# Optimization experiments

Hardware: AMD Instinct MI355X
Metric: run time of the kernel (lower is better)

The kernel has to match this reference:

```python
import jax, jax.numpy as jnp
import numpy as np

DIM = 128
HEADS = 4
K = 7          # neighborhood kernel size
MLP_RATIO = 4
EPS = 1e-5


def setup_inputs() -> dict:
    key = jax.random.key(0)
    ks = jax.random.split(key, 8)
    B, H, W, C = 4, 64, 64, DIM
    hid = C * MLP_RATIO
    s = lambda k, shape: jax.random.normal(k, shape, jnp.float32) * 0.02
    return {
        "x": jax.random.normal(ks[0], (B, H, W, C), jnp.float32),
        "ln1_g": jnp.ones((C,), jnp.float32),
        "ln1_b": jnp.zeros((C,), jnp.float32),
        "qkv_w": s(ks[1], (C, 3 * C)),
        "qkv_b": jnp.zeros((3 * C,), jnp.float32),
        "rpb": s(ks[2], (HEADS, 2 * K - 1, 2 * K - 1)),
        "proj_w": s(ks[3], (C, C)),
        "proj_b": jnp.zeros((C,), jnp.float32),
        "ln2_g": jnp.ones((C,), jnp.float32),
        "ln2_b": jnp.zeros((C,), jnp.float32),
        "fc1_w": s(ks[4], (C, hid)),
        "fc1_b": jnp.zeros((hid,), jnp.float32),
        "fc2_w": s(ks[5], (hid, C)),
        "fc2_b": jnp.zeros((C,), jnp.float32),
    }


def _ln(x, g, b):
    m = jnp.mean(x, axis=-1, keepdims=True)
    v = jnp.mean(jnp.square(x - m), axis=-1, keepdims=True)
    return (x - m) * jax.lax.rsqrt(v + EPS) * g + b


def _neigh_idx(L, k):
    # NATTEN border-clamped neighborhood: start = clamp(i - k//2, 0, L-k)
    i = jnp.arange(L)
    start = jnp.clip(i - k // 2, 0, L - k)
    idx = start[:, None] + jnp.arange(k)[None, :]        # [L, k] key positions
    rel = idx - i[:, None] + (k - 1)                     # [L, k] rpb indices in [0, 2k-2]
    return idx, rel


def _neighborhood_attention(x, qkv_w, qkv_b, rpb, proj_w, proj_b):
    B, H, W, C = x.shape
    nh, hd = HEADS, C // HEADS
    scale = hd ** -0.5
    qkv = (x @ qkv_w + qkv_b).reshape(B, H, W, 3, nh, hd)
    qkv = qkv.transpose(3, 0, 4, 1, 2, 5)                # [3, B, nh, H, W, hd]
    q, k_, v = qkv[0] * scale, qkv[1], qkv[2]
    ih, rh = _neigh_idx(H, K)
    iw, rw = _neigh_idx(W, K)
    # gather 7x7 neighborhoods: [B, nh, H, K, W, K, hd]
    kg = k_[:, :, ih][:, :, :, :, iw]
    vg = v[:, :, ih][:, :, :, :, iw]
    attn = jnp.einsum('bnywc,bnykxjc->bnyxkj', q, kg)    # [B, nh, H, W, K, K]
    bias = rpb[:, rh][:, :, :, rw]                       # [nh, H, K, W, K]
    attn = attn + bias.transpose(0, 1, 3, 2, 4)[None]
    a = jax.nn.softmax(attn.reshape(B, nh, H, W, K * K), axis=-1)
    a = a.reshape(B, nh, H, W, K, K)
    out = jnp.einsum('bnyxkj,bnykxjc->bnyxc', a, vg)     # [B, nh, H, W, hd]
    out = out.transpose(0, 2, 3, 1, 4).reshape(B, H, W, C)
    return out @ proj_w + proj_b


def reference(x, ln1_g, ln1_b, qkv_w, qkv_b, rpb, proj_w, proj_b,
              ln2_g, ln2_b, fc1_w, fc1_b, fc2_w, fc2_b):
    h = x + _neighborhood_attention(_ln(x, ln1_g, ln1_b), qkv_w, qkv_b, rpb, proj_w, proj_b)
    y = _ln(h, ln2_g, ln2_b)
    y = jax.nn.gelu(y @ fc1_w + fc1_b, approximate=False) @ fc2_w + fc2_b
    return h + y
```

## Files before the change

### kernel.cpp

```cpp
#include <hip/hip_runtime.h>
#include <math.h>

#define TOKS 16384
#define CDIM 128
#define NH 4
#define HD 32
#define HID 512
#define QSCALE 0.17677669529663687f
#define LEPS 1e-5f

typedef const float* fp;
typedef const unsigned short* bfp16;
typedef __attribute__((ext_vector_type(8))) short bf16x8;
typedef __attribute__((ext_vector_type(4))) float f32x4;

__device__ inline unsigned int bfp2(float a, float b) {
    unsigned int ua = __float_as_uint(a); ua = (ua + 0x7FFFu + ((ua >> 16) & 1u)) >> 16;
    unsigned int ub = __float_as_uint(b); ub = (ub + 0x7FFFu + ((ub >> 16) & 1u)) >> 16;
    return ua | (ub << 16);
}
__device__ inline unsigned short bf1(float a) {
    unsigned int u = __float_as_uint(a);
    return (unsigned short)((u + 0x7FFFu + ((u >> 16) & 1u)) >> 16);
}
__device__ inline float lo16(unsigned int u) { return __uint_as_float(u << 16); }
__device__ inline float hi16(unsigned int u) { return __uint_as_float(u & 0xFFFF0000u); }

__global__ __launch_bounds__(256) void prep(fp qw, fp pw, fp f1w, fp f2w,
                                            unsigned short* __restrict__ wt) {
    int e = blockIdx.x * 256 + threadIdx.x;
    float v;
    if (e < 49152) { int n = e >> 7, k = e & 127; v = qw[(size_t)k * 384 + n]; }
    else if (e < 65536) {
        int i = e - 49152;
        int frag = i >> 9, w = i & 511, lane = w >> 3, el = w & 7;
        int rt = frag >> 2, kk = frag & 3;
        int row = rt * 16 + (lane & 15);
        int k = kk * 32 + (lane >> 4) * 8 + el;
        v = pw[(size_t)k * 128 + row];
    } else if (e < 131072) {
        int i = e - 65536;
        int frag = i >> 9, w = i & 511, lane = w >> 3, el = w & 7;
        int rt = frag >> 2, kk = frag & 3;
        int row = rt * 16 + (lane & 15);
        int k = kk * 32 + (lane >> 4) * 8 + el;
        v = f1w[(size_t)k * 512 + row];
    } else {
        int i = e - 131072;
        int frag = i >> 9, w = i & 511, lane = w >> 3, el = w & 7;
        int rt = frag >> 4, kc = frag & 15;
        int row = rt * 16 + (lane & 15);
        int k = kc * 32 + (lane >> 4) * 8 + el;
        v = f2w[(size_t)k * 128 + row];
    }
    wt[e] = bf1(v);
}

__global__ __launch_bounds__(256) void k1_mfma(fp x, fp g1, fp b1, bfp16 wt0, fp wb,
                                               float* __restrict__ qb,
                                               unsigned short* __restrict__ kvb) {
    __shared__ unsigned int lds[12288];
    const int m0 = blockIdx.x * 128;
    const int nb = blockIdx.y * 64;
    const int tid = threadIdx.x;
#pragma unroll
    for (int i = 0; i < 8; i++) {
        int slot = tid + i * 256;
        int m = slot >> 4, c16 = slot & 15;
        const float4 v0 = *(const float4*)(x + (size_t)(m0 + m) * CDIM + c16 * 8);
        const float4 v1 = *(const float4*)(x + (size_t)(m0 + m) * CDIM + c16 * 8 + 4);
        float s = v0.x + v0.y + v0.z + v0.w + v1.x + v1.y + v1.z + v1.w;
        float q = v0.x * v0.x + v0.y * v0.y + v0.z * v0.z + v0.w * v0.w
                + v1.x * v1.x + v1.y * v1.y + v1.z * v1.z + v1.w * v1.w;
#pragma unroll
        for (int mm = 8; mm >= 1; mm >>= 1) { s += __shfl_xor(s, mm); q += __shfl_xor(q, mm); }
        float mu = s * (1.f / 128.f);
        float rs = rsqrtf(q * (1.f / 128.f) - mu * mu + LEPS);
        const float4 ga = *(const float4*)(g1 + c16 * 8);
        const float4 gb = *(const float4*)(g1 + c16 * 8 + 4);
        const float4 ba = *(const float4*)(b1 + c16 * 8);
        const float4 bb = *(const float4*)(b1 + c16 * 8 + 4);
        uint4 o;
        o.x = bfp2((v0.x - mu) * rs * ga.x + ba.x, (v0.y - mu) * rs * ga.y + ba.y);
        o.y = bfp2((v0.z - mu) * rs * ga.z + ba.z, (v0.w - mu) * rs * ga.w + ba.w);
        o.z = bfp2((v1.x - mu) * rs * gb.x + bb.x, (v1.y - mu) * rs * gb.y + bb.y);
        o.w = bfp2((v1.z - mu) * rs * gb.z + bb.z, (v1.w - mu) * rs * gb.w + bb.w);
        *(uint4*)&lds[m * 64 + ((c16 ^ (m & 15)) << 2)] = o;
    }
#pragma unroll
    for (int i = 0; i < 4; i++) {
        int slot = tid + i * 256;
        int n = slot >> 4, c16 = slot & 15;
        const uint4 v4 = *(const uint4*)(wt0 + (size_t)(nb + n) * 128 + c16 * 8);
        *(uint4*)&lds[8192 + n * 64 + (c16 ^ (n & 15)) * 4] = v4;
    }
    __syncthreads();

    const int lane = tid & 63, wid = tid >> 6, quad = lane >> 4, l16 = lane & 15;
    f32x4 acc[2][4];
#pragma unroll
    for (int mt = 0; mt < 2; mt++)
#pragma unroll
        for (int nt = 0; nt < 4; nt++) acc[mt][nt] = (f32x4){0.f, 0.f, 0.f, 0.f};
#pragma unroll
    for (int kk = 0; kk < 4; kk++) {
        int c = kk * 4 + quad;
        bf16x8 a0 = *(bf16x8*)&lds[(wid * 32 + l16) * 64 + (c ^ l16) * 4];
        bf16x8 a1 = *(bf16x8*)&lds[(wid * 32 + 16 + l16) * 64 + (c ^ l16) * 4];
#pragma unroll
        for (int nt = 0; nt < 4; nt++) {
            bf16x8 bf = *(bf16x8*)&lds[8192 + (nt * 16 + l16) * 64 + (c ^ l16) * 4];
            acc[0][nt] = __builtin_amdgcn_mfma_f32_16x16x32_bf16(a0, bf, acc[0][nt], 0, 0, 0);
            acc[1][nt] = __builtin_amdgcn_mfma_f32_16x16x32_bf16(a1, bf, acc[1][nt], 0, 0, 0);
        }
    }
#pragma unroll
    for (int nt = 0; nt < 4; nt++) {
        int col = nb + nt * 16 + l16;
        float bias = wb[col];
#pragma unroll
        for (int mt = 0; mt < 2; mt++)
#pragma unroll
            for (int r = 0; r < 4; r++) {
                int row = m0 + wid * 32 + mt * 16 + quad * 4 + r;
                float vres = acc[mt][nt][r] + bias;
                if (col < 128)
                    qb[(size_t)row * 128 + col] = vres * QSCALE;
                else if (col < 256)
                    kvb[(size_t)row * 256 + (col - 128)] = bf1(vres);
                else
                    kvb[(size_t)row * 256 + 128 + (col - 256)] = bf1(vres);
            }
    }
}

__global__ __launch_bounds__(512) void k2_attn(const float* __restrict__ qb,
                                               const unsigned short* __restrict__ kvb,
                                               fp rpb, unsigned short* __restrict__ attnb) {
    __shared__ unsigned int lds[25088];
    const int tile = blockIdx.x;
    const int bb = tile >> 6;
    const int ty0 = ((tile >> 3) & 7) << 3;
    const int tx0 = (tile & 7) << 3;
    const int ry0 = min(max(ty0 - 3, 0), 50);
    const int rx0 = min(max(tx0 - 3, 0), 50);
    const int tid = threadIdx.x;

#pragma unroll
    for (int it = 0; it < 13; it++) {
        int slot = it * 512 + tid;
        if (slot < 6272) {
            int r = slot >> 5, c = slot & 31;
            int i = r / 14, j = r - i * 14;
            const uint4 v = *(const uint4*)(kvb + (size_t)((bb << 12) + (ry0 + i) * 64 + rx0 + j) * 256 + c * 8);
            *(uint4*)&lds[r * 128 + ((c ^ (r & 7)) << 2)] = v;
        }
    }

    const int dh = tid & 1;
    const int head = (tid >> 1) & 3;
    const int t = tid >> 3;
    const int tx = t & 7, ty = t >> 3;
    const int y = ty0 + ty, x = tx0 + tx;
    const int token = (bb << 12) + y * 64 + x;
    const int sy = min(max(y - 3, 0), 57);
    const int sx = min(max(x - 3, 0), 57);
    const int ib = sy - ry0, jb = sx - rx0;
    const float* rp = rpb + head * 169 + (sy - y + 6) * 13 + (sx - x + 6);

    float q[16];
    {
        const float4* qp = (const float4*)(qb + (size_t)token * 128 + head * 32 + dh * 16);
        float4 a = qp[0], b = qp[1], c = qp[2], d = qp[3];
        q[0] = a.x; q[1] = a.y; q[2] = a.z; q[3] = a.w;
        q[4] = b.x; q[5] = b.y; q[6] = b.z; q[7] = b.w;
        q[8] = c.x; q[9] = c.y; q[10] = c.z; q[11] = c.w;
        q[12] = d.x; q[13] = d.y; q[14] = d.z; q[15] = d.w;
    }
    __syncthreads();

    const int cb = (head << 2) + (dh << 1);
    float m = -1e30f, l = 0.f;
    float o[16];
#pragma unroll
    for (int i2 = 0; i2 < 16; i2++) o[i2] = 0.f;

    for (int dy = 0; dy < 7; dy++) {
        float s[7];
#pragma unroll
        for (int dx = 0; dx < 7; dx++) {
            int r = (ib + dy) * 14 + jb + dx;
            int sw = r & 7;
            const uint4 k0 = *(const uint4*)&lds[r * 128 + ((cb ^ sw) << 2)];
            const uint4 k1 = *(const uint4*)&lds[r * 128 + (((cb + 1) ^ sw) << 2)];
            float ss = q[0] * lo16(k0.x) + q[1] * hi16(k0.x)
                     + q[2] * lo16(k0.y) + q[3] * hi16(k0.y)
                     + q[4] * lo16(k0.z) + q[5] * hi16(k0.z)
                     + q[6] * lo16(k0.w) + q[7] * hi16(k0.w)
                     + q[8] * lo16(k1.x) + q[9] * hi16(k1.x)
                     + q[10] * lo16(k1.y) + q[11] * hi16(k1.y)
                     + q[12] * lo16(k1.z) + q[13] * hi16(k1.z)
                     + q[14] * lo16(k1.w) + q[15] * hi16(k1.w);
            ss += __shfl_xor(ss, 1);
            s[dx] = ss + rp[dy * 13 + dx];
        }
        float rm = s[0];
#pragma unroll
        for (int dx = 1; dx < 7; dx++) rm = fmaxf(rm, s[dx]);
        float mn = fmaxf(m, rm);
        float cf = __expf(m - mn);
        l *= cf;
#pragma unroll
        for (int i2 = 0; i2 < 16; i2++) o[i2] *= cf;
#pragma unroll
        for (int dx = 0; dx < 7; dx++) {
            int r = (ib + dy) * 14 + jb + dx;
            int sw = r & 7;
            const uint4 v0 = *(const uint4*)&lds[r * 128 + (((cb + 16) ^ sw) << 2)];
            const uint4 v1 = *(const uint4*)&lds[r * 128 + (((cb + 17) ^ sw) << 2)];
            float p = __expf(s[dx] - mn);
            l += p;
            o[0] += p * lo16(v0.x); o[1] += p * hi16(v0.x);
            o[2] += p * lo16(v0.y); o[3] += p * hi16(v0.y);
            o[4] += p * lo16(v0.z); o[5] += p * hi16(v0.z);
            o[6] += p * lo16(v0.w); o[7] += p * hi16(v0.w);
            o[8] += p * lo16(v1.x); o[9] += p * hi16(v1.x);
            o[10] += p * lo16(v1.y); o[11] += p * hi16(v1.y);
            o[12] += p * lo16(v1.z); o[13] += p * hi16(v1.z);
            o[14] += p * lo16(v1.w); o[15] += p * hi16(v1.w);
        }
        m = mn;
    }
    float inv = 1.f / l;
    unsigned short* op = attnb + (size_t)token * 128 + head * 32 + dh * 16;
    uint4 ov;
    ov.x = bfp2(o[0] * inv, o[1] * inv); ov.y = bfp2(o[2] * inv, o[3] * inv);
    ov.z = bfp2(o[4] * inv, o[5] * inv); ov.w = bfp2(o[6] * inv, o[7] * inv);
    *(uint4*)op = ov;
    ov.x = bfp2(o[8] * inv, o[9] * inv); ov.y = bfp2(o[10] * inv, o[11] * inv);
    ov.z = bfp2(o[12] * inv, o[13] * inv); ov.w = bfp2(o[14] * inv, o[15] * inv);
    *(uint4*)(op + 8) = ov;
}

__global__ __launch_bounds__(512) void kpm4(bfp16 attnb, fp x, bfp16 wt1, fp pb,
                                            fp g2, fp b2, bfp16 wt2, fp b1v,
                                            bfp16 wt3, fp b2v, float* __restrict__ out) {
    __shared__ unsigned int lds[12288];
    float* ldsf = (float*)lds;
    unsigned short* ldsu = (unsigned short*)lds;
    const int m0 = blockIdx.x * 32;
    const int tid = threadIdx.x;
    const int lane = tid & 63, wid = tid >> 6, quad = lane >> 4, l16 = lane & 15;

    {
        int m = tid >> 4, c16 = tid & 15;
        const uint4 v4 = *(const uint4*)(attnb + (size_t)(m0 + m) * CDIM + c16 * 8);
        *(uint4*)&lds[m * 64 + ((c16 ^ (m & 15)) << 2)] = v4;
    }
    __syncthreads();

    const int mt = wid & 1, nhf = wid >> 1;
    f32x4 pacc[2];
#pragma unroll
    for (int nt = 0; nt < 2; nt++) pacc[nt] = (f32x4){0.f, 0.f, 0.f, 0.f};
#pragma unroll
    for (int kk = 0; kk < 4; kk++) {
        int c = kk * 4 + quad;
        bf16x8 a = *(bf16x8*)&lds[(mt * 16 + l16) * 64 + ((c ^ l16) << 2)];
#pragma unroll
        for (int nt = 0; nt < 2; nt++) {
            int rt = nhf * 2 + nt;
            bf16x8 bf = *(const bf16x8*)(wt1 + (size_t)((rt * 4 + kk) * 64 + lane) * 8);
            pacc[nt] = __builtin_amdgcn_mfma_f32_16x16x32_bf16(a, bf, pacc[nt], 0, 0, 0);
        }
    }
    float sr[4] = {0.f, 0.f, 0.f, 0.f}, qr[4] = {0.f, 0.f, 0.f, 0.f};
#pragma unroll
    for (int nt = 0; nt < 2; nt++) {
        int col = nhf * 32 + nt * 16 + l16;
        float bias = pb[col];
#pragma unroll
        for (int r = 0; r < 4; r++) {
            int lrow = mt * 16 + quad * 4 + r;
            float hv = x[(size_t)(m0 + lrow) * CDIM + col] + pacc[nt][r] + bias;
            pacc[nt][r] = hv;
            sr[r] += hv; qr[r] += hv * hv;
        }
    }
#pragma unroll
    for (int mm = 1; mm <= 8; mm <<= 1) {
#pragma unroll
        for (int r = 0; r < 4; r++) {
            sr[r] += __shfl_xor(sr[r], mm);
            qr[r] += __shfl_xor(qr[r], mm);
        }
    }
    __syncthreads();
    if (l16 == 0) {
#pragma unroll
        for (int r = 0; r < 4; r++) {
            ldsf[wid * 32 + (quad * 4 + r) * 2]     = sr[r];
            ldsf[wid * 32 + (quad * 4 + r) * 2 + 1] = qr[r];
        }
    }
    __syncthreads();
    float mu[4], rs[4];
#pragma unroll
    for (int r = 0; r < 4; r++) {
        float st = 0.f, qt = 0.f;
#pragma unroll
        for (int p = 0; p < 4; p++) {
            int w2 = p * 2 + mt;
            st += ldsf[w2 * 32 + (quad * 4 + r) * 2];
            qt += ldsf[w2 * 32 + (quad * 4 + r) * 2 + 1];
        }
        mu[r] = st * (1.f / 128.f);
        rs[r] = rsqrtf(qt * (1.f / 128.f) - mu[r] * mu[r] + LEPS);
    }
#pragma unroll
    for (int nt = 0; nt < 2; nt++) {
        int col = nhf * 32 + nt * 16 + l16;
        float gg = g2[col], bbv = b2[col];
        int c16h = col >> 3, cw = col & 7;
#pragma unroll
        for (int r = 0; r < 4; r++) {
            int lrow = mt * 16 + quad * 4 + r;
            ldsu[4096 + lrow * 128 + ((c16h ^ (lrow & 15)) << 3) + cw] =
                bf1((pacc[nt][r] - mu[r]) * rs[r] * gg + bbv);
        }
    }
    __syncthreads();

#pragma unroll
    for (int ht = 0; ht < 4; ht++) {
        f32x4 acc0 = (f32x4){0.f, 0.f, 0.f, 0.f};
        f32x4 acc1 = (f32x4){0.f, 0.f, 0.f, 0.f};
#pragma unroll
        for (int kk = 0; kk < 4; kk++) {
            int c = kk * 4 + quad;
            bf16x8 wf = *(const bf16x8*)(wt2 + (size_t)(((wid * 4 + ht) * 4 + kk) * 64 + lane) * 8);
            bf16x8 x0 = *(bf16x8*)&lds[2048 + l16 * 64 + ((c ^ l16) << 2)];
            bf16x8 x1 = *(bf16x8*)&lds[2048 + (16 + l16) * 64 + ((c ^ l16) << 2)];
            acc0 = __builtin_amdgcn_mfma_f32_16x16x32_bf16(wf, x0, acc0, 0, 0, 0);
            acc1 = __builtin_amdgcn_mfma_f32_16x16x32_bf16(wf, x1, acc1, 0, 0, 0);
        }
        const int hidb = wid * 64 + ht * 16 + quad * 4;
        const float4 bb = *(const float4*)(b1v + hidb);
        const int c16y = hidb >> 3;
        const int woff = (quad & 1) << 1;
#pragma unroll
        for (int t = 0; t < 2; t++) {
            f32x4 a = t ? acc1 : acc0;
            int row = t * 16 + l16;
            float z0 = a[0] + bb.x, z1 = a[1] + bb.y, z2 = a[2] + bb.z, z3 = a[3] + bb.w;
            float g0 = 0.5f * z0 * (1.f + erff(z0 * 0.70710678118654752f));
            float g1 = 0.5f * z1 * (1.f + erff(z1 * 0.70710678118654752f));
            float g2v = 0.5f * z2 * (1.f + erff(z2 * 0.70710678118654752f));
            float g3 = 0.5f * z3 * (1.f + erff(z3 * 0.70710678118654752f));
            uint2 val; val.x = bfp2(g0, g1); val.y = bfp2(g2v, g3);
            *(uint2*)&lds[4096 + row * 256 + ((c16y ^ (row & 15)) << 2) + woff] = val;
        }
    }
    __syncthreads();

    f32x4 facc[2];
#pragma unroll
    for (int nt = 0; nt < 2; nt++) facc[nt] = (f32x4){0.f, 0.f, 0.f, 0.f};
#pragma unroll
    for (int kc = 0; kc < 16; kc++) {
        int c = kc * 4 + quad;
        bf16x8 a = *(bf16x8*)&lds[4096 + (mt * 16 + l16) * 256 + ((c ^ l16) << 2)];
#pragma unroll
        for (int nt = 0; nt < 2; nt++) {
            int rt = nhf * 2 + nt;
            bf16x8 bf = *(const bf16x8*)(wt3 + (size_t)((rt * 16 + kc) * 64 + lane) * 8);
            facc[nt] = __builtin_amdgcn_mfma_f32_16x16x32_bf16(a, bf, facc[nt], 0, 0, 0);
        }
    }
#pragma unroll
    for (int nt = 0; nt < 2; nt++) {
        int col = nhf * 32 + nt * 16 + l16;
        float bias = b2v[col];
#pragma unroll
        for (int r = 0; r < 4; r++) {
            int lrow = mt * 16 + quad * 4 + r;
            out[(size_t)(m0 + lrow) * CDIM + col] = pacc[nt][r] + facc[nt][r] + bias;
        }
    }
}

extern "C" void kernel_launch(void* const* d_in, const int* in_sizes, int n_in,
                              void* d_out, int out_size, void* d_ws, size_t ws_size,
                              hipStream_t stream) {
    fp x      = (fp)d_in[0];
    fp ln1_g  = (fp)d_in[1];
    fp ln1_b  = (fp)d_in[2];
    fp qkv_w  = (fp)d_in[3];
    fp qkv_b  = (fp)d_in[4];
    fp rpb    = (fp)d_in[5];
    fp proj_w = (fp)d_in[6];
    fp proj_b = (fp)d_in[7];
    fp ln2_g  = (fp)d_in[8];
    fp ln2_b  = (fp)d_in[9];
    fp fc1_w  = (fp)d_in[10];
    fp fc1_b  = (fp)d_in[11];
    fp fc2_w  = (fp)d_in[12];
    fp fc2_b  = (fp)d_in[13];
    float* out = (float*)d_out;

    float* ws = (float*)d_ws;
    float* h  = ws;
    unsigned short* xn = (unsigned short*)(h + (size_t)TOKS * CDIM);
    unsigned short* hn = xn + (size_t)TOKS * CDIM;
    float* qb = (float*)(hn + (size_t)TOKS * CDIM);
    unsigned short* kvb   = (unsigned short*)(qb + (size_t)TOKS * CDIM);
    unsigned short* attnb = kvb + (size_t)TOKS * 256;
    unsigned short* wt    = attnb + (size_t)TOKS * CDIM;

    unsigned short* wt0 = wt;
    unsigned short* wt1 = wt + 49152;
    unsigned short* wt2 = wt + 65536;
    unsigned short* wt3 = wt + 131072;

    prep<<<768, 256, 0, stream>>>(qkv_w, proj_w, fc1_w, fc2_w, wt);
    k1_mfma<<<dim3(TOKS / 128, 6), 256, 0, stream>>>(x, ln1_g, ln1_b, wt0, qkv_b, qb, kvb);
    k2_attn<<<TOKS / 64, 512, 0, stream>>>(qb, kvb, rpb, attnb);
    kpm4<<<TOKS / 32, 512, 0, stream>>>(attnb, x, wt1, proj_b, ln2_g, ln2_b,
                                        wt2, fc1_b, wt3, fc2_b, out);
}
```

Measured before the change: 130.8 us.

## Split attention blocks by head pairs and use two-pass softmax

```diff
diff --git a/kernel.cpp b/kernel.cpp
--- a/kernel.cpp
+++ b/kernel.cpp
@@ -134,11 +134,13 @@
     }
 }
 
-__global__ __launch_bounds__(512) void k2_attn(const float* __restrict__ qb,
+__global__ __launch_bounds__(256) void k2_attn(const float* __restrict__ qb,
                                                const unsigned short* __restrict__ kvb,
                                                fp rpb, unsigned short* __restrict__ attnb) {
-    __shared__ unsigned int lds[25088];
-    const int tile = blockIdx.x;
+    __shared__ unsigned int lds[12544];
+    const int blk = blockIdx.x;
+    const int hp = blk & 1;
+    const int tile = blk >> 1;
     const int bb = tile >> 6;
     const int ty0 = ((tile >> 3) & 7) << 3;
     const int tx0 = (tile & 7) << 3;
@@ -148,18 +150,21 @@
 
 #pragma unroll
     for (int it = 0; it < 13; it++) {
-        int slot = it * 512 + tid;
-        if (slot < 6272) {
-            int r = slot >> 5, c = slot & 31;
+        int slot = it * 256 + tid;
+        if (slot < 3136) {
+            int r = slot >> 4, c = slot & 15;
             int i = r / 14, j = r - i * 14;
-            const uint4 v = *(const uint4*)(kvb + (size_t)((bb << 12) + (ry0 + i) * 64 + rx0 + j) * 256 + c * 8);
-            *(uint4*)&lds[r * 128 + ((c ^ (r & 7)) << 2)] = v;
+            size_t tok = (size_t)((bb << 12) + (ry0 + i) * 64 + rx0 + j);
+            int off = (c < 8) ? (hp * 64 + c * 8) : (128 + hp * 64 + (c - 8) * 8);
+            const uint4 v = *(const uint4*)(kvb + tok * 256 + off);
+            *(uint4*)&lds[r * 64 + ((c ^ (r & 7)) << 2)] = v;
         }
     }
 
     const int dh = tid & 1;
-    const int head = (tid >> 1) & 3;
-    const int t = tid >> 3;
+    const int hl = (tid >> 1) & 1;
+    const int t = tid >> 2;
+    const int head = hp * 2 + hl;
     const int tx = t & 7, ty = t >> 3;
     const int y = ty0 + ty, x = tx0 + tx;
     const int token = (bb << 12) + y * 64 + x;
@@ -167,6 +172,8 @@
     const int sx = min(max(x - 3, 0), 57);
     const int ib = sy - ry0, jb = sx - rx0;
     const float* rp = rpb + head * 169 + (sy - y + 6) * 13 + (sx - x + 6);
+    const int cbK = hl * 4 + dh * 2;
+    const int cbV = 8 + cbK;
 
     float q[16];
     {
@@ -179,20 +186,16 @@
     }
     __syncthreads();
 
-    const int cb = (head << 2) + (dh << 1);
-    float m = -1e30f, l = 0.f;
-    float o[16];
-#pragma unroll
-    for (int i2 = 0; i2 < 16; i2++) o[i2] = 0.f;
-
+    float s[49];
+    float mx = -1e30f;
+#pragma unroll
     for (int dy = 0; dy < 7; dy++) {
-        float s[7];
 #pragma unroll
         for (int dx = 0; dx < 7; dx++) {
             int r = (ib + dy) * 14 + jb + dx;
             int sw = r & 7;
-            const uint4 k0 = *(const uint4*)&lds[r * 128 + ((cb ^ sw) << 2)];
-            const uint4 k1 = *(const uint4*)&lds[r * 128 + (((cb + 1) ^ sw) << 2)];
+            const uint4 k0 = *(const uint4*)&lds[r * 64 + ((cbK ^ sw) << 2)];
+            const uint4 k1 = *(const uint4*)&lds[r * 64 + (((cbK + 1) ^ sw) << 2)];
             float ss = q[0] * lo16(k0.x) + q[1] * hi16(k0.x)
                      + q[2] * lo16(k0.y) + q[3] * hi16(k0.y)
                      + q[4] * lo16(k0.z) + q[5] * hi16(k0.z)
@@ -202,24 +205,28 @@
                      + q[12] * lo16(k1.z) + q[13] * hi16(k1.z)
                      + q[14] * lo16(k1.w) + q[15] * hi16(k1.w);
             ss += __shfl_xor(ss, 1);
-            s[dx] = ss + rp[dy * 13 + dx];
-        }
-        float rm = s[0];
-#pragma unroll
-        for (int dx = 1; dx < 7; dx++) rm = fmaxf(rm, s[dx]);
-        float mn = fmaxf(m, rm);
-        float cf = __expf(m - mn);
-        l *= cf;
-#pragma unroll
-        for (int i2 = 0; i2 < 16; i2++) o[i2] *= cf;
+            float sc = ss + rp[dy * 13 + dx];
+            s[dy * 7 + dx] = sc;
+            mx = fmaxf(mx, sc);
+        }
+    }
+    float sum = 0.f;
+#pragma unroll
+    for (int i = 0; i < 49; i++) { s[i] = __expf(s[i] - mx); sum += s[i]; }
+    float inv = 1.f / sum;
+
+    float o[16];
+#pragma unroll
+    for (int i2 = 0; i2 < 16; i2++) o[i2] = 0.f;
+#pragma unroll
+    for (int dy = 0; dy < 7; dy++) {
 #pragma unroll
         for (int dx = 0; dx < 7; dx++) {
             int r = (ib + dy) * 14 + jb + dx;
             int sw = r & 7;
-            const uint4 v0 = *(const uint4*)&lds[r * 128 + (((cb + 16) ^ sw) << 2)];
-            const uint4 v1 = *(const uint4*)&lds[r * 128 + (((cb + 17) ^ sw) << 2)];
-            float p = __expf(s[dx] - mn);
-            l += p;
+            const uint4 v0 = *(const uint4*)&lds[r * 64 + ((cbV ^ sw) << 2)];
+            const uint4 v1 = *(const uint4*)&lds[r * 64 + (((cbV + 1) ^ sw) << 2)];
+            float p = s[dy * 7 + dx];
             o[0] += p * lo16(v0.x); o[1] += p * hi16(v0.x);
             o[2] += p * lo16(v0.y); o[3] += p * hi16(v0.y);
             o[4] += p * lo16(v0.z); o[5] += p * hi16(v0.z);
@@ -229,9 +236,7 @@
             o[12] += p * lo16(v1.z); o[13] += p * hi16(v1.z);
             o[14] += p * lo16(v1.w); o[15] += p * hi16(v1.w);
         }
-        m = mn;
-    }
-    float inv = 1.f / l;
+    }
     unsigned short* op = attnb + (size_t)token * 128 + head * 32 + dh * 16;
     uint4 ov;
     ov.x = bfp2(o[0] * inv, o[1] * inv); ov.y = bfp2(o[2] * inv, o[3] * inv);
@@ -424,7 +429,7 @@
 
     prep<<<768, 256, 0, stream>>>(qkv_w, proj_w, fc1_w, fc2_w, wt);
     k1_mfma<<<dim3(TOKS / 128, 6), 256, 0, stream>>>(x, ln1_g, ln1_b, wt0, qkv_b, qb, kvb);
-    k2_attn<<<TOKS / 64, 512, 0, stream>>>(qb, kvb, rpb, attnb);
+    k2_attn<<<TOKS / 64 * 2, 256, 0, stream>>>(qb, kvb, rpb, attnb);
     kpm4<<<TOKS / 32, 512, 0, stream>>>(attnb, x, wt1, proj_b, ln2_g, ln2_b,
                                         wt2, fc1_b, wt3, fc2_b, out);
 }
```

After: 131.9 us. About the same (+0.8%).

## Fuse weight-prep kernel into QKV kernel and convert QKV weights in-block

Applied to the files above, without the earlier changes.

```diff
diff --git a/kernel.cpp b/kernel.cpp
--- a/kernel.cpp
+++ b/kernel.cpp
@@ -26,43 +26,45 @@
 __device__ inline float lo16(unsigned int u) { return __uint_as_float(u << 16); }
 __device__ inline float hi16(unsigned int u) { return __uint_as_float(u & 0xFFFF0000u); }
 
-__global__ __launch_bounds__(256) void prep(fp qw, fp pw, fp f1w, fp f2w,
-                                            unsigned short* __restrict__ wt) {
-    int e = blockIdx.x * 256 + threadIdx.x;
-    float v;
-    if (e < 49152) { int n = e >> 7, k = e & 127; v = qw[(size_t)k * 384 + n]; }
-    else if (e < 65536) {
-        int i = e - 49152;
-        int frag = i >> 9, w = i & 511, lane = w >> 3, el = w & 7;
-        int rt = frag >> 2, kk = frag & 3;
-        int row = rt * 16 + (lane & 15);
-        int k = kk * 32 + (lane >> 4) * 8 + el;
-        v = pw[(size_t)k * 128 + row];
-    } else if (e < 131072) {
-        int i = e - 65536;
-        int frag = i >> 9, w = i & 511, lane = w >> 3, el = w & 7;
-        int rt = frag >> 2, kk = frag & 3;
-        int row = rt * 16 + (lane & 15);
-        int k = kk * 32 + (lane >> 4) * 8 + el;
-        v = f1w[(size_t)k * 512 + row];
-    } else {
-        int i = e - 131072;
-        int frag = i >> 9, w = i & 511, lane = w >> 3, el = w & 7;
-        int rt = frag >> 4, kc = frag & 15;
-        int row = rt * 16 + (lane & 15);
-        int k = kc * 32 + (lane >> 4) * 8 + el;
-        v = f2w[(size_t)k * 128 + row];
-    }
-    wt[e] = bf1(v);
-}
-
-__global__ __launch_bounds__(256) void k1_mfma(fp x, fp g1, fp b1, bfp16 wt0, fp wb,
+__global__ __launch_bounds__(256) void k1_mfma(fp x, fp g1, fp b1, fp qw, fp wb,
+                                               fp pw, fp f1w, fp f2w,
+                                               unsigned short* __restrict__ wt,
                                                float* __restrict__ qb,
                                                unsigned short* __restrict__ kvb) {
+    const int blk = blockIdx.x;
+    const int tid = threadIdx.x;
+    if (blk >= 768) {
+        int e = 49152 + (blk - 768) * 256 + tid;
+        float v;
+        if (e < 65536) {
+            int i = e - 49152;
+            int frag = i >> 9, w = i & 511, lane = w >> 3, el = w & 7;
+            int rt = frag >> 2, kk = frag & 3;
+            int row = rt * 16 + (lane & 15);
+            int k = kk * 32 + (lane >> 4) * 8 + el;
+            v = pw[(size_t)k * 128 + row];
+        } else if (e < 131072) {
+            int i = e - 65536;
+            int frag = i >> 9, w = i & 511, lane = w >> 3, el = w & 7;
+            int rt = frag >> 2, kk = frag & 3;
+            int row = rt * 16 + (lane & 15);
+            int k = kk * 32 + (lane >> 4) * 8 + el;
+            v = f1w[(size_t)k * 512 + row];
+        } else {
+            int i = e - 131072;
+            int frag = i >> 9, w = i & 511, lane = w >> 3, el = w & 7;
+            int rt = frag >> 4, kc = frag & 15;
+            int row = rt * 16 + (lane & 15);
+            int k = kc * 32 + (lane >> 4) * 8 + el;
+            v = f2w[(size_t)k * 128 + row];
+        }
+        wt[e] = bf1(v);
+        return;
+    }
+
     __shared__ unsigned int lds[12288];
-    const int m0 = blockIdx.x * 128;
-    const int nb = blockIdx.y * 64;
-    const int tid = threadIdx.x;
+    const int m0 = (blk & 127) << 7;
+    const int nb = (blk >> 7) * 64;
 #pragma unroll
     for (int i = 0; i < 8; i++) {
         int slot = tid + i * 256;
@@ -87,12 +89,25 @@
         o.w = bfp2((v1.z - mu) * rs * gb.z + bb.z, (v1.w - mu) * rs * gb.w + bb.w);
         *(uint4*)&lds[m * 64 + ((c16 ^ (m & 15)) << 2)] = o;
     }
-#pragma unroll
-    for (int i = 0; i < 4; i++) {
-        int slot = tid + i * 256;
-        int n = slot >> 4, c16 = slot & 15;
-        const uint4 v4 = *(const uint4*)(wt0 + (size_t)(nb + n) * 128 + c16 * 8);
-        *(uint4*)&lds[8192 + n * 64 + (c16 ^ (n & 15)) * 4] = v4;
+    {
+        const int k4 = tid >> 3;
+        const int no = tid & 7;
+        float rw[4][8];
+#pragma unroll
+        for (int e4 = 0; e4 < 4; e4++) {
+            const float* src = qw + (size_t)(k4 * 4 + e4) * 384 + nb + no * 8;
+            *(float4*)&rw[e4][0] = *(const float4*)src;
+            *(float4*)&rw[e4][4] = *(const float4*)(src + 4);
+        }
+        const int c16 = k4 >> 1, half = k4 & 1;
+#pragma unroll
+        for (int j = 0; j < 8; j++) {
+            int n = no * 8 + j;
+            uint2 pk;
+            pk.x = bfp2(rw[0][j], rw[1][j]);
+            pk.y = bfp2(rw[2][j], rw[3][j]);
+            *(uint2*)&lds[8192 + n * 64 + ((c16 ^ (n & 15)) << 2) + half * 2] = pk;
+        }
     }
     __syncthreads();
 
@@ -417,13 +432,12 @@
     unsigned short* attnb = kvb + (size_t)TOKS * 256;
     unsigned short* wt    = attnb + (size_t)TOKS * CDIM;
 
-    unsigned short* wt0 = wt;
     unsigned short* wt1 = wt + 49152;
     unsigned short* wt2 = wt + 65536;
     unsigned short* wt3 = wt + 131072;
 
-    prep<<<768, 256, 0, stream>>>(qkv_w, proj_w, fc1_w, fc2_w, wt);
-    k1_mfma<<<dim3(TOKS / 128, 6), 256, 0, stream>>>(x, ln1_g, ln1_b, wt0, qkv_b, qb, kvb);
+    k1_mfma<<<768 + 576, 256, 0, stream>>>(x, ln1_g, ln1_b, qkv_w, qkv_b,
+                                           proj_w, fc1_w, fc2_w, wt, qb, kvb);
     k2_attn<<<TOKS / 64, 512, 0, stream>>>(qb, kvb, rpb, attnb);
     kpm4<<<TOKS / 32, 512, 0, stream>>>(attnb, x, wt1, proj_b, ln2_g, ln2_b,
                                         wt2, fc1_b, wt3, fc2_b, out);
```

Measured after the change: 130.9 us, median of 2. No clear change (+0.0%).
